# Optimization experiments

Hardware: AMD Instinct MI355X
Metric: run time of the kernel (lower is better)

Reference implementation:

```python
import jax, jax.numpy as jnp
import numpy as np

B, T, D_IN, D_OUT = 4, 2048, 1024, 1024


def setup_inputs() -> dict:
    key = jax.random.key(0)
    k0, k1, k2, k3 = jax.random.split(key, 4)
    token_embed = jax.random.normal(k0, (B, T, D_IN), dtype=jnp.float32)
    # torch Linear weight is [out, in]; store transposed [in, out] for x @ W
    Wq = jax.random.normal(k1, (D_IN, D_OUT), dtype=jnp.float32) * (1.0 / np.sqrt(D_IN))
    Wk = jax.random.normal(k2, (D_IN, D_OUT), dtype=jnp.float32) * (1.0 / np.sqrt(D_IN))
    Wv = jax.random.normal(k3, (D_IN, D_OUT), dtype=jnp.float32) * (1.0 / np.sqrt(D_IN))
    return {"token_embed": token_embed, "Wq": Wq, "Wk": Wk, "Wv": Wv}


def reference(token_embed, Wq, Wk, Wv):
    # token_embed: [B, T, d_in]
    num_token = token_embed.shape[1]
    q = jnp.einsum("btd,de->bte", token_embed, Wq)  # [B, T, d_out]
    k = jnp.einsum("btd,de->bte", token_embed, Wk)
    v = jnp.einsum("btd,de->bte", token_embed, Wv)
    scores = jnp.einsum("bqe,bke->bqk", q, k)  # [B, T, T]
    # causal mask: strictly-upper-triangular positions set to -inf
    causal = jnp.triu(jnp.ones((num_token, num_token), dtype=bool), k=1)
    scores = jnp.where(causal[None, :, :], -jnp.inf, scores)
    # NOTE: faithful to source bug: scale by sqrt(seq_len) (keys.shape[1]), not sqrt(d_out)
    scale = jnp.asarray(num_token, dtype=scores.dtype) ** 0.5
    attn = jax.nn.softmax(scores / scale, axis=-1)
    # dropout prob is 0 -> identity
    context = jnp.einsum("bqk,bke->bqe", attn, v)  # [B, T, d_out]
    return context
```

## Files before the change

### kernel.cpp

```cpp
#include <hip/hip_runtime.h>
#include <cstdint>
#include <cstddef>
#include <math.h>


typedef __attribute__((ext_vector_type(4))) float f32x4;
typedef __attribute__((ext_vector_type(8))) short s16x8;

#define AS1(p) ((const __attribute__((address_space(1))) void*)(p))
#define AS3(p) ((__attribute__((address_space(3))) void*)(p))
#define BARRIER() asm volatile("s_barrier" ::: "memory")
#define W8 asm volatile("s_waitcnt vmcnt(8)" ::: "memory")
#define W4 asm volatile("s_waitcnt vmcnt(4)" ::: "memory")
#define W0 asm volatile("s_waitcnt vmcnt(0)" ::: "memory")
#define WNONE ((void)0)
#define NOISSUE ((void)0)

static __device__ __forceinline__ unsigned short f2bf(float x) {
  unsigned int u = __float_as_uint(x);
  unsigned int r = u + 0x7FFFu + ((u >> 16) & 1u);
  return (unsigned short)(r >> 16);
}
static __device__ __forceinline__ float bf2f(unsigned short h) {
  return __uint_as_float(((unsigned int)h) << 16);
}

__global__ __launch_bounds__(256) void k_cvt(const float* __restrict__ X,
                                             const float* __restrict__ W0p,
                                             const float* __restrict__ W1p,
                                             const float* __restrict__ W2p,
                                             unsigned short* __restrict__ Xb,
                                             unsigned short* __restrict__ Wt) {
  __shared__ float tile[64][65];
  const int bx = blockIdx.x;
  if (bx < 4096) {
    size_t i = ((size_t)bx * 256 + threadIdx.x) * 8;
    float4 a = *(const float4*)(X + i);
    float4 b = *(const float4*)(X + i + 4);
    union { unsigned short us[8]; uint4 v; } o;
    o.us[0] = f2bf(a.x); o.us[1] = f2bf(a.y); o.us[2] = f2bf(a.z); o.us[3] = f2bf(a.w);
    o.us[4] = f2bf(b.x); o.us[5] = f2bf(b.y); o.us[6] = f2bf(b.z); o.us[7] = f2bf(b.w);
    *(uint4*)(Xb + i) = o.v;
    return;
  }
  const int bx2 = bx - 4096;
  const int z = bx2 >> 8, t = bx2 & 255;
  const float* W = z == 0 ? W0p : (z == 1 ? W1p : W2p);
  unsigned short* dst = Wt + (size_t)z * 1048576;
  const int k0 = (t >> 4) * 64, n0 = (t & 15) * 64;
  const int tr = threadIdx.x >> 4, tc = (threadIdx.x & 15) * 4;
  for (int i = 0; i < 4; ++i) {
    int r = tr + i * 16;
    float4 v = *(const float4*)(W + (size_t)(k0 + r) * 1024 + n0 + tc);
    tile[r][tc + 0] = v.x; tile[r][tc + 1] = v.y;
    tile[r][tc + 2] = v.z; tile[r][tc + 3] = v.w;
  }
  __syncthreads();
  for (int i = 0; i < 4; ++i) {
    int r = tr + i * 16;
    ushort4 o;
    o.x = f2bf(tile[tc + 0][r]); o.y = f2bf(tile[tc + 1][r]);
    o.z = f2bf(tile[tc + 2][r]); o.w = f2bf(tile[tc + 3][r]);
    *(ushort4*)(dst + (size_t)(n0 + r) * 1024 + k0 + tc) = o;
  }
}

static __device__ __forceinline__ void stage2(const char* src, size_t ld128, char* dst) {
  __builtin_amdgcn_global_load_lds(AS1(src), AS3(dst), 16, 0, 0);
  __builtin_amdgcn_global_load_lds(AS1(src + ld128), AS3(dst + 8192), 16, 0, 0);
}

template <class FA, class FB>
static __device__ __forceinline__ void core256(const char* __restrict__ As,
                                               const char* __restrict__ Bs,
                                               size_t ldA128, size_t ldB128,
                                               FA offA, FB offB,
                                               int nkt, char* smem, f32x4 (&acc)[8][4]) {
  const int tid = threadIdx.x, w = tid >> 6, lane = tid & 63;
  const int lr = lane & 15, lq = lane >> 4;
  const int wm = (w >> 2) * 128, wn = (w & 3) * 64;
  char* ldsA = smem + w * 1024;
  char* ldsB = smem + 65536 + w * 1024;
  s16x8 af[4], bfr[4];

#define STG_A(t, h) stage2(As + offA((t), (h)), ldA128, ldsA + (((t) & 1) * 2 + (h)) * 16384)
#define STG_B(t, h) stage2(Bs + offB((t), (h)), ldB128, ldsB + (((t) & 1) * 2 + (h)) * 16384)
#define RD_A(buf, h, r) (*(const s16x8*)(smem + ((buf) * 2 + (h)) * 16384 + (r) * 64 + ((lq ^ (((r) >> 1) & 3)) << 4)))
#define RD_B(buf, h, r) (*(const s16x8*)(smem + 65536 + ((buf) * 2 + (h)) * 16384 + (r) * 64 + ((lq ^ (((r) >> 1) & 3)) << 4)))
#define ISS_H1(T) do { STG_A((T) + 1, 1); STG_B((T) + 1, 1); } while (0)
#define ISS_H0(T) do { STG_A((T) + 2, 0); STG_B((T) + 2, 0); } while (0)
#define MFMA_Q(base)                                                                     \
  _Pragma("unroll") for (int i = 0; i < 4; ++i)                                          \
  _Pragma("unroll") for (int c = 0; c < 4; ++c)                                          \
    acc[(base) + i][c] = __builtin_amdgcn_mfma_f32_16x16x32_bf16(af[i], bfr[c], acc[(base) + i][c], 0, 0, 0)
#define PH02(buf, h, ISSUE)                                                              \
  _Pragma("unroll") for (int i = 0; i < 4; ++i) af[i] = RD_A(buf, h, wm + i * 16 + lr);  \
  _Pragma("unroll") for (int c = 0; c < 4; ++c) bfr[c] = RD_B(buf, h, wn + c * 16 + lr); \
  ISSUE; BARRIER();                                                                      \
  __builtin_amdgcn_s_setprio(1); MFMA_Q(0); __builtin_amdgcn_s_setprio(0);               \
  BARRIER();
#define PH13(buf, h, WAIT)                                                               \
  _Pragma("unroll") for (int i = 0; i < 4; ++i) af[i] = RD_A(buf, h, wm + 64 + i * 16 + lr); \
  BARRIER();                                                                             \
  __builtin_amdgcn_s_setprio(1); MFMA_Q(4); __builtin_amdgcn_s_setprio(0);               \
  WAIT; BARRIER();
#define TILE(T, ISS0, ISS2, WAIT1, WAIT3) {                                              \
    const int _buf = (T) & 1;                                                            \
    PH02(_buf, 0, ISS0)                                                                  \
    PH13(_buf, 0, WAIT1)                                                                 \
    PH02(_buf, 1, ISS2)                                                                  \
    PH13(_buf, 1, WAIT3)                                                                 \
  }

  STG_A(0, 0); STG_B(0, 0);
  STG_A(0, 1); STG_B(0, 1);
  STG_A(1, 0); STG_B(1, 0);
  W8; BARRIER();

  int t = 0;
  for (; t + 2 < nkt; ++t) TILE(t, ISS_H1(t), ISS_H0(t), W8, W8)
  TILE(t, ISS_H1(t), NOISSUE, W8, W4)
  ++t;
  TILE(t, NOISSUE, NOISSUE, W0, WNONE)

#undef STG_A
#undef STG_B
#undef RD_A
#undef RD_B
#undef ISS_H1
#undef ISS_H0
#undef MFMA_Q
#undef PH02
#undef PH13
#undef TILE
}

struct OffLinear {
  __device__ __forceinline__ size_t operator()(int t, int h) const {
    return (size_t)t * 128 + (size_t)h * 64;
  }
};
struct OffTriK {
  int k0;
  __device__ __forceinline__ size_t operator()(int t, int h) const {
    int g = k0 + t;
    return (size_t)(g >> 2) * 131072 + (size_t)(g & 3) * 128 + (size_t)h * 64;
  }
};
struct OffLinK {
  int k0;
  __device__ __forceinline__ size_t operator()(int t, int h) const {
    return (size_t)(k0 + t) * 128 + (size_t)h * 64;
  }
};

static __device__ __forceinline__ void lane_src(int& rowl, int& slot) {
  const int tid = threadIdx.x, w = tid >> 6, lane = tid & 63;
  rowl = w * 16 + (lane >> 2);
  slot = (lane & 3) ^ ((rowl >> 1) & 3);
}

__global__ __launch_bounds__(512, 2) void k_qk(const unsigned short* __restrict__ Xb,
                                               const unsigned short* __restrict__ Wt,
                                               unsigned short* __restrict__ Qm,
                                               unsigned short* __restrict__ Km) {
  __shared__ char smem[131072];
  const int by = blockIdx.y, z = by >> 2, q = by & 3, bx = blockIdx.x;
  const int m0 = bx * 256, n0 = q * 256;
  const char* A = (const char*)(Xb + (size_t)m0 * 1024);
  const char* B = (const char*)(Wt + (size_t)z * 1048576 + (size_t)n0 * 1024);
  int rowl, slot; lane_src(rowl, slot);
  const size_t lo = (size_t)rowl * 2048 + slot * 16;
  f32x4 acc[8][4];
#pragma unroll
  for (int i = 0; i < 8; ++i)
#pragma unroll
    for (int c = 0; c < 4; ++c) acc[i][c] = (f32x4){0.f, 0.f, 0.f, 0.f};
  core256(A + lo, B + lo, (size_t)128 * 2048, (size_t)128 * 2048,
          OffLinear{}, OffLinear{}, 16, smem, acc);
  unsigned short* C = z == 0 ? Qm : Km;
  const int tid = threadIdx.x, w = tid >> 6, lane = tid & 63;
  const int lr = lane & 15, lq = lane >> 4;
  const int wm = (w >> 2) * 128, wn = (w & 3) * 64;
#pragma unroll
  for (int fr = 0; fr < 8; ++fr)
#pragma unroll
    for (int fc = 0; fc < 4; ++fc)
#pragma unroll
      for (int i = 0; i < 4; ++i) {
        int row = m0 + wm + fr * 16 + lq * 4 + i;
        int col = n0 + wn + fc * 16 + lr;
        C[(size_t)row * 1024 + col] = f2bf(acc[fr][fc][i]);
      }
}

__global__ __launch_bounds__(512, 2) void k_v(const unsigned short* __restrict__ Xb,
                                              const unsigned short* __restrict__ Wt,
                                              unsigned short* __restrict__ Vt) {
  __shared__ char smem[131072];
  const int x = blockIdx.x;
  const int m0 = (x & 3) * 256, n0 = (x >> 2) * 256;
  const char* A = (const char*)(Wt + (size_t)2 * 1048576 + (size_t)m0 * 1024);
  const char* B = (const char*)(Xb + (size_t)n0 * 1024);
  int rowl, slot; lane_src(rowl, slot);
  const size_t lo = (size_t)rowl * 2048 + slot * 16;
  f32x4 acc[8][4];
#pragma unroll
  for (int a = 0; a < 8; ++a)
#pragma unroll
    for (int c = 0; c < 4; ++c) acc[a][c] = (f32x4){0.f, 0.f, 0.f, 0.f};
  core256(A + lo, B + lo, (size_t)128 * 2048, (size_t)128 * 2048,
          OffLinear{}, OffLinear{}, 16, smem, acc);
  const int tid = threadIdx.x, w = tid >> 6, lane = tid & 63;
  const int lr = lane & 15, lq = lane >> 4;
  const int wm = (w >> 2) * 128, wn = (w & 3) * 64;
#pragma unroll
  for (int fr = 0; fr < 8; ++fr)
#pragma unroll
    for (int fc = 0; fc < 4; ++fc)
#pragma unroll
      for (int i = 0; i < 4; ++i) {
        int row = m0 + wm + fr * 16 + lq * 4 + i;
        int col = n0 + wn + fc * 16 + lr;
        Vt[((size_t)(col >> 11) * 1024 + row) * 2048 + (col & 2047)] = f2bf(acc[fr][fc][i]);
      }
}

__global__ __launch_bounds__(512, 2) void k_sg(const unsigned short* __restrict__ Qm,
                                               const unsigned short* __restrict__ Km,
                                               unsigned short* __restrict__ S) {
  __shared__ char smem[131072];
  const int id = blockIdx.x;
  int i = 0;
  while ((i + 1) * (i + 2) / 2 <= id) ++i;
  const int j = id - i * (i + 1) / 2;
  const int b = blockIdx.y;
  const int m0 = i * 256, n0 = j * 256;
  int rowl, slot; lane_src(rowl, slot);
  const size_t lo = (size_t)rowl * 2048 + slot * 16;
  f32x4 acc[8][4];
#pragma unroll
  for (int a = 0; a < 8; ++a)
#pragma unroll
    for (int c = 0; c < 4; ++c) acc[a][c] = (f32x4){0.f, 0.f, 0.f, 0.f};
  core256((const char*)(Qm + ((size_t)b * 2048 + m0) * 1024) + lo,
          (const char*)(Km + ((size_t)b * 2048 + n0) * 1024) + lo,
          (size_t)128 * 2048, (size_t)128 * 2048, OffLinear{}, OffLinear{}, 16, smem, acc);
  const float SCALE = 0.022097086912079608f;
  const int tid = threadIdx.x, w = tid >> 6, lane = tid & 63;
  const int lr = lane & 15, lq = lane >> 4;
  const int wm = (w >> 2) * 128, wn = (w & 3) * 64;
  unsigned short* tb = S + (((size_t)(b * 36 + id)) << 16);
#pragma unroll
  for (int fr = 0; fr < 8; ++fr)
#pragma unroll
    for (int fc = 0; fc < 4; ++fc)
#pragma unroll
      for (int i2 = 0; i2 < 4; ++i2) {
        int rl = wm + fr * 16 + lq * 4 + i2;
        int cl = wn + fc * 16 + lr;
        tb[(size_t)rl * 256 + cl] = f2bf(acc[fr][fc][i2] * SCALE);
      }
}

__global__ __launch_bounds__(256) void k_softmax(unsigned short* __restrict__ S) {
  const int tid = threadIdx.x, w = tid >> 6, lane = tid & 63;
  const int row = blockIdx.x * 4 + w;
  const int b = row >> 11, q = row & 2047;
  const int i = q >> 8, ntl = i + 1, rowL = q & 255;
  unsigned short* base = S + (((size_t)(b * 36 + (i * (i + 1)) / 2)) << 16)
                           + (size_t)rowL * 256 + lane * 4;
  float v[8][4];
#pragma unroll
  for (int t = 0; t < 8; ++t) {
    if (t < ntl) {
      ushort4 x = *(const ushort4*)(base + (size_t)t * 65536);
      int c0 = t * 256 + lane * 4;
      v[t][0] = (c0 + 0 <= q) ? bf2f(x.x) : -INFINITY;
      v[t][1] = (c0 + 1 <= q) ? bf2f(x.y) : -INFINITY;
      v[t][2] = (c0 + 2 <= q) ? bf2f(x.z) : -INFINITY;
      v[t][3] = (c0 + 3 <= q) ? bf2f(x.w) : -INFINITY;
    } else {
      v[t][0] = v[t][1] = v[t][2] = v[t][3] = -INFINITY;
    }
  }
  float m = -INFINITY;
#pragma unroll
  for (int t = 0; t < 8; ++t)
#pragma unroll
    for (int jj = 0; jj < 4; ++jj) m = fmaxf(m, v[t][jj]);
  for (int off = 32; off; off >>= 1) m = fmaxf(m, __shfl_xor(m, off));
  float s = 0.f;
#pragma unroll
  for (int t = 0; t < 8; ++t)
#pragma unroll
    for (int jj = 0; jj < 4; ++jj) { v[t][jj] = __expf(v[t][jj] - m); s += v[t][jj]; }
  for (int off = 32; off; off >>= 1) s += __shfl_xor(s, off);
  const float inv = 1.f / s;
#pragma unroll
  for (int t = 0; t < 8; ++t)
    if (t < ntl) {
      ushort4 o;
      o.x = f2bf(v[t][0] * inv); o.y = f2bf(v[t][1] * inv);
      o.z = f2bf(v[t][2] * inv); o.w = f2bf(v[t][3] * inv);
      *(ushort4*)(base + (size_t)t * 65536) = o;
    }
}

__device__ const int pvi[15] = {2, 5, 5, 7, 7, 4, 4, 6, 7, 6, 6, 1, 3, 3, 0};
__device__ const int pvk[15] = {0, 0, 12, 0, 11, 0, 10, 0, 22, 10, 19, 0, 0, 8, 0};
__device__ const int pvn[15] = {12, 12, 12, 11, 11, 10, 10, 10, 10, 9, 9, 8, 8, 8, 4};
__device__ const int pvp[15] = {-1, -1, 2, -1, 5, -1, 1, -1, 6, 3, 4, -1, -1, 0, -1};

__global__ __launch_bounds__(512, 2) void k_pv(const unsigned short* __restrict__ P,
                                               const unsigned short* __restrict__ Vt,
                                               float* __restrict__ out,
                                               float* __restrict__ part) {
  __shared__ char smem[131072];
  const int cx = blockIdx.x % 15;
  const int panel = blockIdx.x / 15;
  const int nt = panel & 3, b = panel >> 2;
  const int i = pvi[cx], k0 = pvk[cx], nkt = pvn[cx], psl = pvp[cx];
  const char* Pb = (const char*)P + (((size_t)(b * 36 + (i * (i + 1)) / 2)) << 17);
  int rowl, slot; lane_src(rowl, slot);
  const char* Asrc = Pb + (size_t)rowl * 512 + slot * 16;
  const char* Bsrc = (const char*)Vt + ((size_t)(b * 1024 + nt * 256 + rowl)) * 4096 + slot * 16;
  f32x4 acc[8][4];
#pragma unroll
  for (int a = 0; a < 8; ++a)
#pragma unroll
    for (int c = 0; c < 4; ++c) acc[a][c] = (f32x4){0.f, 0.f, 0.f, 0.f};
  core256(Asrc, Bsrc, (size_t)128 * 512, (size_t)128 * 4096,
          OffTriK{k0}, OffLinK{k0}, nkt, smem, acc);
  const int tid = threadIdx.x, w = tid >> 6, lane = tid & 63;
  const int lr = lane & 15, lq = lane >> 4;
  const int wm = (w >> 2) * 128, wn = (w & 3) * 64;
  if (psl < 0) {
#pragma unroll
    for (int fr = 0; fr < 8; ++fr)
#pragma unroll
      for (int fc = 0; fc < 4; ++fc)
#pragma unroll
        for (int i2 = 0; i2 < 4; ++i2) {
          int orow = i * 256 + wm + fr * 16 + lq * 4 + i2;
          int col = nt * 256 + wn + fc * 16 + lr;
          out[((size_t)b * 2048 + orow) * 1024 + col] = acc[fr][fc][i2];
        }
  } else {
    float* pt = part + ((size_t)(panel * 7 + psl)) * 65536;
#pragma unroll
    for (int fr = 0; fr < 8; ++fr)
#pragma unroll
      for (int fc = 0; fc < 4; ++fc)
#pragma unroll
        for (int i2 = 0; i2 < 4; ++i2) {
          int rl = wm + fr * 16 + lq * 4 + i2;
          int cl = wn + fc * 16 + lr;
          pt[(size_t)rl * 256 + cl] = acc[fr][fc][i2];
        }
  }
}

__global__ __launch_bounds__(256) void k_fix(float* __restrict__ out,
                                             const float* __restrict__ part) {
  const size_t e = ((size_t)blockIdx.x * 256 + threadIdx.x) * 4;
  const int b = (int)(e / 1310720);
  const int rem = (int)(e % 1310720);
  const int row = 768 + (rem >> 10);
  const int col = rem & 1023;
  const int i = row >> 8;
  const int nt = col >> 8;
  const int base4[5] = {0, 1, 2, 3, 5};
  const int cnt4[5] = {1, 1, 1, 2, 2};
  const int sb = base4[i - 3], cnt = cnt4[i - 3];
  const float* pt = part + ((size_t)((b * 4 + nt) * 7 + sb)) * 65536
                         + (size_t)(row & 255) * 256 + (col & 255);
  float* op = out + ((size_t)b * 2048 + row) * 1024 + col;
  float4 o = *(const float4*)op;
  float4 p0 = *(const float4*)pt;
  o.x += p0.x; o.y += p0.y; o.z += p0.z; o.w += p0.w;
  if (cnt == 2) {
    float4 p1 = *(const float4*)(pt + 65536);
    o.x += p1.x; o.y += p1.y; o.z += p1.z; o.w += p1.w;
  }
  *(float4*)op = o;
}

extern "C" void kernel_launch(void* const* d_in, const int* in_sizes, int n_in,
                              void* d_out, int out_size, void* d_ws, size_t ws_size,
                              hipStream_t stream) {
  const float* X  = (const float*)d_in[0];
  const float* W0p = (const float*)d_in[1];
  const float* W1p = (const float*)d_in[2];
  const float* W2p = (const float*)d_in[3];
  float* out = (float*)d_out;
  char* ws = (char*)d_ws;
  unsigned short* Xb = (unsigned short*)ws;
  unsigned short* Wt = (unsigned short*)(ws + (size_t)16777216);
  unsigned short* Qm = (unsigned short*)(ws + (size_t)23068672);
  unsigned short* Km = (unsigned short*)(ws + (size_t)39845888);
  unsigned short* Vt = (unsigned short*)(ws + (size_t)56623104);
  unsigned short* Sb = (unsigned short*)ws;
  float* Pp = (float*)(ws + (size_t)23068672);
  (void)in_sizes; (void)n_in; (void)out_size; (void)ws_size;

  hipLaunchKernelGGL(k_cvt, dim3(4864), dim3(256), 0, stream, X, W0p, W1p, W2p, Xb, Wt);
  hipLaunchKernelGGL(k_qk, dim3(32, 8), dim3(512), 0, stream, Xb, Wt, Qm, Km);
  hipLaunchKernelGGL(k_v, dim3(128), dim3(512), 0, stream, Xb, Wt, Vt);
  hipLaunchKernelGGL(k_sg, dim3(36, 4), dim3(512), 0, stream, Qm, Km, Sb);
  hipLaunchKernelGGL(k_softmax, dim3(2048), dim3(256), 0, stream, Sb);
  hipLaunchKernelGGL(k_pv, dim3(240), dim3(512), 0, stream, Sb, Vt, out, Pp);
  hipLaunchKernelGGL(k_fix, dim3(5120), dim3(256), 0, stream, out, Pp);
}
```

Baseline: 170.1 us.

## Double-buffer MFMA operand fragments so LDS reads overlap matrix math

The GEMM inner loop now keeps two sets of A and B fragment registers. Fragments for the next phase are read from LDS while the MFMA block runs on the previous set, including a prefetch of the next k-tile's first half at the end of each tile. The vmcnt waits move earlier, to just after the phases that issue global-to-LDS loads. This is meant to hide LDS read latency behind MFMA work, at the cost of roughly 32 extra VGPRs per thread, which may lower occupancy or cause spills.

```diff
diff --git a/kernel.cpp b/kernel.cpp
--- a/kernel.cpp
+++ b/kernel.cpp
@@ -81,41 +81,39 @@
   const int wm = (w >> 2) * 128, wn = (w & 3) * 64;
   char* ldsA = smem + w * 1024;
   char* ldsB = smem + 65536 + w * 1024;
-  s16x8 af[4], bfr[4];
+  s16x8 aA[4], aB[4], bA[4], bB[4];
 
 #define STG_A(t, h) stage2(As + offA((t), (h)), ldA128, ldsA + (((t) & 1) * 2 + (h)) * 16384)
 #define STG_B(t, h) stage2(Bs + offB((t), (h)), ldB128, ldsB + (((t) & 1) * 2 + (h)) * 16384)
 #define RD_A(buf, h, r) (*(const s16x8*)(smem + ((buf) * 2 + (h)) * 16384 + (r) * 64 + ((lq ^ (((r) >> 1) & 3)) << 4)))
 #define RD_B(buf, h, r) (*(const s16x8*)(smem + 65536 + ((buf) * 2 + (h)) * 16384 + (r) * 64 + ((lq ^ (((r) >> 1) & 3)) << 4)))
+#define RD_ALO(dst, buf, h) \
+  _Pragma("unroll") for (int i = 0; i < 4; ++i) dst[i] = RD_A(buf, h, wm + i * 16 + lr);
+#define RD_AHI(dst, buf, h) \
+  _Pragma("unroll") for (int i = 0; i < 4; ++i) dst[i] = RD_A(buf, h, wm + 64 + i * 16 + lr);
+#define RD_BF(dst, buf, h) \
+  _Pragma("unroll") for (int c = 0; c < 4; ++c) dst[c] = RD_B(buf, h, wn + c * 16 + lr);
 #define ISS_H1(T) do { STG_A((T) + 1, 1); STG_B((T) + 1, 1); } while (0)
 #define ISS_H0(T) do { STG_A((T) + 2, 0); STG_B((T) + 2, 0); } while (0)
-#define MFMA_Q(base)                                                                     \
-  _Pragma("unroll") for (int i = 0; i < 4; ++i)                                          \
-  _Pragma("unroll") for (int c = 0; c < 4; ++c)                                          \
-    acc[(base) + i][c] = __builtin_amdgcn_mfma_f32_16x16x32_bf16(af[i], bfr[c], acc[(base) + i][c], 0, 0, 0)
-#define PH02(buf, h, ISSUE)                                                              \
-  _Pragma("unroll") for (int i = 0; i < 4; ++i) af[i] = RD_A(buf, h, wm + i * 16 + lr);  \
-  _Pragma("unroll") for (int c = 0; c < 4; ++c) bfr[c] = RD_B(buf, h, wn + c * 16 + lr); \
-  ISSUE; BARRIER();                                                                      \
-  __builtin_amdgcn_s_setprio(1); MFMA_Q(0); __builtin_amdgcn_s_setprio(0);               \
-  BARRIER();
-#define PH13(buf, h, WAIT)                                                               \
-  _Pragma("unroll") for (int i = 0; i < 4; ++i) af[i] = RD_A(buf, h, wm + 64 + i * 16 + lr); \
-  BARRIER();                                                                             \
-  __builtin_amdgcn_s_setprio(1); MFMA_Q(4); __builtin_amdgcn_s_setprio(0);               \
-  WAIT; BARRIER();
-#define TILE(T, ISS0, ISS2, WAIT1, WAIT3) {                                              \
-    const int _buf = (T) & 1;                                                            \
-    PH02(_buf, 0, ISS0)                                                                  \
-    PH13(_buf, 0, WAIT1)                                                                 \
-    PH02(_buf, 1, ISS2)                                                                  \
-    PH13(_buf, 1, WAIT3)                                                                 \
+#define MM(AF, BF, base) \
+  __builtin_amdgcn_s_setprio(1); \
+  _Pragma("unroll") for (int i = 0; i < 4; ++i) \
+  _Pragma("unroll") for (int c = 0; c < 4; ++c) \
+    acc[(base) + i][c] = __builtin_amdgcn_mfma_f32_16x16x32_bf16(AF[i], BF[c], acc[(base) + i][c], 0, 0, 0); \
+  __builtin_amdgcn_s_setprio(0);
+#define TILE(T, ISS0, ISS2, WT0, WT2) { \
+    const int _b = (T) & 1; \
+    RD_AHI(aB, _b, 0); ISS0; BARRIER(); MM(aA, bA, 0); WT0; BARRIER(); \
+    RD_ALO(aA, _b, 1); RD_BF(bB, _b, 1); BARRIER(); MM(aB, bA, 4); BARRIER(); \
+    RD_AHI(aB, _b, 1); ISS2; BARRIER(); MM(aA, bB, 0); WT2; BARRIER(); \
+    RD_ALO(aA, 1 - _b, 0); RD_BF(bA, 1 - _b, 0); BARRIER(); MM(aB, bB, 4); BARRIER(); \
   }
 
   STG_A(0, 0); STG_B(0, 0);
   STG_A(0, 1); STG_B(0, 1);
   STG_A(1, 0); STG_B(1, 0);
   W8; BARRIER();
+  RD_ALO(aA, 0, 0); RD_BF(bA, 0, 0);
 
   int t = 0;
   for (; t + 2 < nkt; ++t) TILE(t, ISS_H1(t), ISS_H0(t), W8, W8)
@@ -127,11 +125,12 @@
 #undef STG_B
 #undef RD_A
 #undef RD_B
+#undef RD_ALO
+#undef RD_AHI
+#undef RD_BF
 #undef ISS_H1
 #undef ISS_H0
-#undef MFMA_Q
-#undef PH02
-#undef PH13
+#undef MM
 #undef TILE
 }
 
```

New measurement: 173.2 us. Within noise of the previous version (+1.8%).
